# Kernel optimization log

Measured on AMD Instinct MI355X. Metric: run time of the kernel, lower is better.

## Reference

```python
import jax, jax.numpy as jnp
import numpy as np

EPS = 1e-8  # torch F.cosine_similarity eps


def setup_inputs() -> dict:
    key = jax.random.key(0)
    k1, k2 = jax.random.split(key)
    B, D = 8192, 512
    return {
        "label_tensor": jnp.arange(B, dtype=jnp.int64),
        "feature_a": jax.random.normal(k1, (B, D), dtype=jnp.float32),
        "feature_b": jax.random.normal(k2, (B, D), dtype=jnp.float32),
        "affine_w": jnp.ones((1,), dtype=jnp.float32),   # AffineModel scale
        "affine_b": jnp.zeros((1,), dtype=jnp.float32),  # AffineModel bias
    }


def reference(label_tensor, feature_a, feature_b, affine_w, affine_b):
    # cos_score[i, j] = cos(a_i, b_j): normalize then one [B,D]x[D,B] GEMM
    a_n = feature_a / jnp.maximum(
        jnp.linalg.norm(feature_a, axis=1, keepdims=True), EPS)
    b_n = feature_b / jnp.maximum(
        jnp.linalg.norm(feature_b, axis=1, keepdims=True), EPS)
    cos_score = jnp.einsum("id,jd->ij", a_n, b_n)  # [B, B]
    cos_score = affine_w[0] * cos_score + affine_b[0]  # AffineModel
    # cross-entropy with labels = arange(B) -> diagonal of log_softmax
    logp = jax.nn.log_softmax(cos_score, axis=1)
    B = cos_score.shape[0]
    loss = -jnp.mean(logp[jnp.arange(B), jnp.arange(B)])
    return (loss, cos_score)
```

## Files before the change

kernel.cpp:

```cpp
#include <hip/hip_runtime.h>
#include <hip/hip_bf16.h>

#define B_ROWS 8192
#define DIM 512

typedef __bf16 bf16x8 __attribute__((ext_vector_type(8)));
typedef float f32x4 __attribute__((ext_vector_type(4)));

__device__ inline ushort f2bf(float x) {
    __hip_bfloat16 h = __float2bfloat16(x);
    return __builtin_bit_cast(ushort, h);
}

__global__ __launch_bounds__(256) void norm_kernel(const float* __restrict__ A,
                                                   const float* __restrict__ Bf,
                                                   ushort* __restrict__ An,
                                                   ushort* __restrict__ Bn) {
    int gw = (blockIdx.x * 256 + threadIdx.x) >> 6;
    int lane = threadIdx.x & 63;
    const float* src;
    ushort* dst;
    if (gw < B_ROWS) {
        src = A + (size_t)gw * DIM;
        dst = An + (size_t)gw * DIM;
    } else {
        src = Bf + (size_t)(gw - B_ROWS) * DIM;
        dst = Bn + (size_t)(gw - B_ROWS) * DIM;
    }
    const float4* s4 = (const float4*)src;
    float4 v0 = s4[lane * 2];
    float4 v1 = s4[lane * 2 + 1];
    float ss = v0.x * v0.x + v0.y * v0.y + v0.z * v0.z + v0.w * v0.w
             + v1.x * v1.x + v1.y * v1.y + v1.z * v1.z + v1.w * v1.w;
#pragma unroll
    for (int m = 32; m >= 1; m >>= 1) ss += __shfl_xor(ss, m, 64);
    float scale = 1.0f / fmaxf(sqrtf(ss), 1e-8f);
    union { ushort us[8]; uint4 q; } o;
    o.us[0] = f2bf(v0.x * scale); o.us[1] = f2bf(v0.y * scale);
    o.us[2] = f2bf(v0.z * scale); o.us[3] = f2bf(v0.w * scale);
    o.us[4] = f2bf(v1.x * scale); o.us[5] = f2bf(v1.y * scale);
    o.us[6] = f2bf(v1.z * scale); o.us[7] = f2bf(v1.w * scale);
    ((uint4*)dst)[lane] = o.q;
}

__global__ __launch_bounds__(256, 2) void gemm_kernel(
    const ushort* __restrict__ An, const ushort* __restrict__ Bn,
    float* __restrict__ C, float* __restrict__ row_sum,
    const float* __restrict__ wp, const float* __restrict__ bp) {
    __shared__ ushort lds[8192];

    const int t = threadIdx.x;
    const int brow = blockIdx.y * 128;
    const int bcol = blockIdx.x * 128;
    const int wid = t >> 6, lane = t & 63;
    const int wr = wid >> 1, wc = wid & 1;

    const int sr = t >> 2;
    const int sc = (t & 3) * 8;
    const ushort* gA = An + (size_t)(brow + sr) * DIM + sc;
    const ushort* gB = Bn + (size_t)(bcol + sr) * DIM + sc;
    ushort* lA = &lds[t * 8];
    ushort* lB = &lds[4096 + t * 8];

    f32x4 acc[4][4];
#pragma unroll
    for (int i = 0; i < 4; i++)
#pragma unroll
        for (int j = 0; j < 4; j++) acc[i][j] = (f32x4){0.f, 0.f, 0.f, 0.f};

    const int fr = lane & 15;
    const int fk = (lane >> 4) * 8;

    for (int kt = 0; kt < DIM / 32; ++kt) {
        const int k0 = kt * 32;
        __syncthreads();
        __builtin_amdgcn_global_load_lds(
            (const __attribute__((address_space(1))) unsigned int*)(gA + k0),
            (__attribute__((address_space(3))) unsigned int*)lA, 16, 0, 0);
        __builtin_amdgcn_global_load_lds(
            (const __attribute__((address_space(1))) unsigned int*)(gA + (size_t)64 * DIM + k0),
            (__attribute__((address_space(3))) unsigned int*)(lA + 2048), 16, 0, 0);
        __builtin_amdgcn_global_load_lds(
            (const __attribute__((address_space(1))) unsigned int*)(gB + k0),
            (__attribute__((address_space(3))) unsigned int*)lB, 16, 0, 0);
        __builtin_amdgcn_global_load_lds(
            (const __attribute__((address_space(1))) unsigned int*)(gB + (size_t)64 * DIM + k0),
            (__attribute__((address_space(3))) unsigned int*)(lB + 2048), 16, 0, 0);
        __syncthreads();

        bf16x8 af[4], bfr[4];
#pragma unroll
        for (int m = 0; m < 4; ++m) {
            int row = wr * 64 + m * 16 + fr;
            af[m] = *(const bf16x8*)&lds[row * 32 + fk];
        }
#pragma unroll
        for (int n = 0; n < 4; ++n) {
            int col = wc * 64 + n * 16 + fr;
            bfr[n] = *(const bf16x8*)&lds[4096 + col * 32 + fk];
        }
#pragma unroll
        for (int m = 0; m < 4; ++m)
#pragma unroll
            for (int n = 0; n < 4; ++n)
                acc[m][n] = __builtin_amdgcn_mfma_f32_16x16x32_bf16(af[m], bfr[n], acc[m][n], 0, 0, 0);
    }

    const float w = wp[0], bb = bp[0];
    const float M = fabsf(w) + fabsf(bb);
#pragma unroll
    for (int m = 0; m < 4; ++m) {
#pragma unroll
        for (int r = 0; r < 4; ++r) {
            int grow = brow + wr * 64 + m * 16 + (lane >> 4) * 4 + r;
            float psum = 0.f;
#pragma unroll
            for (int n = 0; n < 4; ++n) {
                int gcol = bcol + wc * 64 + n * 16 + (lane & 15);
                float s = w * acc[m][n][r] + bb;
                C[(size_t)grow * B_ROWS + gcol] = s;
                psum += __expf(s - M);
            }
#pragma unroll
            for (int msk = 1; msk <= 8; msk <<= 1) psum += __shfl_xor(psum, msk, 64);
            if ((lane & 15) == 0) atomicAdd(&row_sum[grow], psum);
        }
    }
}

__global__ __launch_bounds__(1024) void loss_kernel(const float* __restrict__ C,
                                                    const float* __restrict__ row_sum,
                                                    const float* __restrict__ wp,
                                                    const float* __restrict__ bp,
                                                    float* __restrict__ out0) {
    __shared__ float sred[16];
    float M = fabsf(wp[0]) + fabsf(bp[0]);
    float local = 0.f;
    for (int i = threadIdx.x; i < B_ROWS; i += 1024) {
        float sii = C[(size_t)i * (B_ROWS + 1)];
        local += sii - M - __logf(row_sum[i]);
    }
#pragma unroll
    for (int m = 32; m >= 1; m >>= 1) local += __shfl_xor(local, m, 64);
    if ((threadIdx.x & 63) == 0) sred[threadIdx.x >> 6] = local;
    __syncthreads();
    if (threadIdx.x == 0) {
        float tot = 0.f;
        for (int i = 0; i < 16; ++i) tot += sred[i];
        out0[0] = -tot / (float)B_ROWS;
    }
}

extern "C" void kernel_launch(void* const* d_in, const int* in_sizes, int n_in,
                              void* d_out, int out_size, void* d_ws, size_t ws_size,
                              hipStream_t stream) {
    const float* A  = (const float*)d_in[1];
    const float* Bf = (const float*)d_in[2];
    const float* wp = (const float*)d_in[3];
    const float* bp = (const float*)d_in[4];
    float* out = (float*)d_out;

    ushort* An = (ushort*)d_ws;
    ushort* Bn = An + (size_t)B_ROWS * DIM;
    float* row_sum = (float*)((char*)d_ws + (size_t)2 * B_ROWS * DIM * sizeof(ushort));

    hipMemsetAsync(row_sum, 0, B_ROWS * sizeof(float), stream);
    norm_kernel<<<dim3(16384 * 64 / 256), 256, 0, stream>>>(A, Bf, An, Bn);
    dim3 grid(B_ROWS / 128, B_ROWS / 128);
    gemm_kernel<<<grid, 256, 0, stream>>>(An, Bn, out + 1, row_sum, wp, bp);
    loss_kernel<<<1, 1024, 0, stream>>>(out + 1, row_sum, wp, bp, out);
}
```

Measured before the change: 437.2 us.

## Use 256x256 double-buffered swizzled GEMM tiles and deterministic row-sum partials

Enlarges the GEMM block tile to 256x256 with 512 threads and double-buffers the LDS tiles, prefetching the next k-slice while MFMAs run. It adds an XOR swizzle on LDS chunks to cut bank conflicts and raises wave priority around the MFMA block. Per-row exp sums are reduced in shared memory and written as per-column-block partials instead of using global atomics. The loss kernel then runs across many blocks and combines results with one atomic per block. The cost is more registers and LDS per block, which may lower occupancy, plus an extra partials buffer.

Measured after the change: 397.7 us. 9.0% less time.

```diff
diff --git a/kernel.cpp b/kernel.cpp
--- a/kernel.cpp
+++ b/kernel.cpp
@@ -43,111 +43,121 @@
     ((uint4*)dst)[lane] = o.q;
 }
 
-__global__ __launch_bounds__(256, 2) void gemm_kernel(
+#define GLDS(src, dst) __builtin_amdgcn_global_load_lds( \
+    (const __attribute__((address_space(1))) unsigned int*)(src), \
+    (__attribute__((address_space(3))) unsigned int*)(dst), 16, 0, 0)
+
+__global__ __launch_bounds__(512, 2) void gemm_kernel(
     const ushort* __restrict__ An, const ushort* __restrict__ Bn,
-    float* __restrict__ C, float* __restrict__ row_sum,
+    float* __restrict__ C, float* __restrict__ rowpart,
     const float* __restrict__ wp, const float* __restrict__ bp) {
-    __shared__ ushort lds[8192];
+    __shared__ ushort ldsA[2][8192];
+    __shared__ ushort ldsB[2][8192];
 
     const int t = threadIdx.x;
-    const int brow = blockIdx.y * 128;
-    const int bcol = blockIdx.x * 128;
+    const int brow = blockIdx.y * 256;
+    const int bcol = blockIdx.x * 256;
     const int wid = t >> 6, lane = t & 63;
-    const int wr = wid >> 1, wc = wid & 1;
+    const int wr = wid >> 2, wc = wid & 3;
+    const int fr = lane & 15;
+    const int fhi = lane >> 4;
 
-    const int sr = t >> 2;
-    const int sc = (t & 3) * 8;
-    const ushort* gA = An + (size_t)(brow + sr) * DIM + sc;
-    const ushort* gB = Bn + (size_t)(bcol + sr) * DIM + sc;
-    ushort* lA = &lds[t * 8];
-    ushort* lB = &lds[4096 + t * 8];
+    const int srow = t >> 2;
+    const int schunk = (t & 3) ^ ((t >> 3) & 3);
+    const ushort* gA0 = An + (size_t)(brow + srow) * DIM + schunk * 8;
+    const ushort* gA1 = gA0 + (size_t)128 * DIM;
+    const ushort* gB0 = Bn + (size_t)(bcol + srow) * DIM + schunk * 8;
+    const ushort* gB1 = gB0 + (size_t)128 * DIM;
 
-    f32x4 acc[4][4];
+#define STAGE(buf, kt) do { const int k0_ = (kt) * 32;            \
+        GLDS(gA0 + k0_, &ldsA[buf][t * 8]);                       \
+        GLDS(gA1 + k0_, &ldsA[buf][4096 + t * 8]);                \
+        GLDS(gB0 + k0_, &ldsB[buf][t * 8]);                       \
+        GLDS(gB1 + k0_, &ldsB[buf][4096 + t * 8]); } while (0)
+
+    f32x4 acc[8][4];
 #pragma unroll
-    for (int i = 0; i < 4; i++)
+    for (int i = 0; i < 8; i++)
 #pragma unroll
         for (int j = 0; j < 4; j++) acc[i][j] = (f32x4){0.f, 0.f, 0.f, 0.f};
 
-    const int fr = lane & 15;
-    const int fk = (lane >> 4) * 8;
+    const int rchunk = (fhi ^ ((fr >> 1) & 3)) * 8;
 
-    for (int kt = 0; kt < DIM / 32; ++kt) {
-        const int k0 = kt * 32;
-        __syncthreads();
-        __builtin_amdgcn_global_load_lds(
-            (const __attribute__((address_space(1))) unsigned int*)(gA + k0),
-            (__attribute__((address_space(3))) unsigned int*)lA, 16, 0, 0);
-        __builtin_amdgcn_global_load_lds(
-            (const __attribute__((address_space(1))) unsigned int*)(gA + (size_t)64 * DIM + k0),
-            (__attribute__((address_space(3))) unsigned int*)(lA + 2048), 16, 0, 0);
-        __builtin_amdgcn_global_load_lds(
-            (const __attribute__((address_space(1))) unsigned int*)(gB + k0),
-            (__attribute__((address_space(3))) unsigned int*)lB, 16, 0, 0);
-        __builtin_amdgcn_global_load_lds(
-            (const __attribute__((address_space(1))) unsigned int*)(gB + (size_t)64 * DIM + k0),
-            (__attribute__((address_space(3))) unsigned int*)(lB + 2048), 16, 0, 0);
-        __syncthreads();
+    STAGE(0, 0);
+    __syncthreads();
 
-        bf16x8 af[4], bfr[4];
+    int cur = 0;
 #pragma unroll
-        for (int m = 0; m < 4; ++m) {
-            int row = wr * 64 + m * 16 + fr;
-            af[m] = *(const bf16x8*)&lds[row * 32 + fk];
-        }
+    for (int kt = 0; kt < 16; ++kt) {
+        if (kt < 15) STAGE(cur ^ 1, kt + 1);
+        bf16x8 af[8], bfr[4];
 #pragma unroll
-        for (int n = 0; n < 4; ++n) {
-            int col = wc * 64 + n * 16 + fr;
-            bfr[n] = *(const bf16x8*)&lds[4096 + col * 32 + fk];
-        }
+        for (int m = 0; m < 8; ++m)
+            af[m] = *(const bf16x8*)&ldsA[cur][(wr * 128 + m * 16 + fr) * 32 + rchunk];
 #pragma unroll
-        for (int m = 0; m < 4; ++m)
+        for (int n = 0; n < 4; ++n)
+            bfr[n] = *(const bf16x8*)&ldsB[cur][(wc * 64 + n * 16 + fr) * 32 + rchunk];
+        __builtin_amdgcn_s_setprio(1);
+#pragma unroll
+        for (int m = 0; m < 8; ++m)
 #pragma unroll
             for (int n = 0; n < 4; ++n)
                 acc[m][n] = __builtin_amdgcn_mfma_f32_16x16x32_bf16(af[m], bfr[n], acc[m][n], 0, 0, 0);
+        __builtin_amdgcn_s_setprio(0);
+        __syncthreads();
+        cur ^= 1;
     }
 
     const float w = wp[0], bb = bp[0];
     const float M = fabsf(w) + fabsf(bb);
+    float* part = (float*)&ldsA[0][0];
 #pragma unroll
-    for (int m = 0; m < 4; ++m) {
+    for (int m = 0; m < 8; ++m) {
 #pragma unroll
         for (int r = 0; r < 4; ++r) {
-            int grow = brow + wr * 64 + m * 16 + (lane >> 4) * 4 + r;
+            const int rloc = wr * 128 + m * 16 + fhi * 4 + r;
+            const size_t grow = (size_t)(brow + rloc);
             float psum = 0.f;
 #pragma unroll
             for (int n = 0; n < 4; ++n) {
-                int gcol = bcol + wc * 64 + n * 16 + (lane & 15);
-                float s = w * acc[m][n][r] + bb;
-                C[(size_t)grow * B_ROWS + gcol] = s;
+                const int gcol = bcol + wc * 64 + n * 16 + fr;
+                float s = fmaf(w, acc[m][n][r], bb);
+                C[grow * B_ROWS + gcol] = s;
                 psum += __expf(s - M);
             }
 #pragma unroll
             for (int msk = 1; msk <= 8; msk <<= 1) psum += __shfl_xor(psum, msk, 64);
-            if ((lane & 15) == 0) atomicAdd(&row_sum[grow], psum);
+            if (fr == 0) part[wc * 256 + rloc] = psum;
         }
     }
+    __syncthreads();
+    if (t < 256) {
+        float s = part[t] + part[256 + t] + part[512 + t] + part[768 + t];
+        rowpart[(size_t)blockIdx.x * B_ROWS + brow + t] = s;
+    }
+#undef STAGE
 }
 
-__global__ __launch_bounds__(1024) void loss_kernel(const float* __restrict__ C,
-                                                    const float* __restrict__ row_sum,
-                                                    const float* __restrict__ wp,
-                                                    const float* __restrict__ bp,
-                                                    float* __restrict__ out0) {
-    __shared__ float sred[16];
-    float M = fabsf(wp[0]) + fabsf(bp[0]);
-    float local = 0.f;
-    for (int i = threadIdx.x; i < B_ROWS; i += 1024) {
-        float sii = C[(size_t)i * (B_ROWS + 1)];
-        local += sii - M - __logf(row_sum[i]);
-    }
+__global__ __launch_bounds__(256) void loss_kernel(const float* __restrict__ C,
+                                                   const float* __restrict__ rowpart,
+                                                   const float* __restrict__ wp,
+                                                   const float* __restrict__ bp,
+                                                   float* __restrict__ out0) {
+    __shared__ float sred[4];
+    const int row = blockIdx.x * 256 + threadIdx.x;
+    float rs = 0.f;
 #pragma unroll
-    for (int m = 32; m >= 1; m >>= 1) local += __shfl_xor(local, m, 64);
-    if ((threadIdx.x & 63) == 0) sred[threadIdx.x >> 6] = local;
+    for (int j = 0; j < 32; ++j) rs += rowpart[(size_t)j * B_ROWS + row];
+    const float M = fabsf(wp[0]) + fabsf(bp[0]);
+    const float sii = C[(size_t)row * B_ROWS + row];
+    float v = sii - M - __logf(rs);
+#pragma unroll
+    for (int msk = 32; msk >= 1; msk >>= 1) v += __shfl_xor(v, msk, 64);
+    if ((threadIdx.x & 63) == 0) sred[threadIdx.x >> 6] = v;
     __syncthreads();
     if (threadIdx.x == 0) {
-        float tot = 0.f;
-        for (int i = 0; i < 16; ++i) tot += sred[i];
-        out0[0] = -tot / (float)B_ROWS;
+        float tot = sred[0] + sred[1] + sred[2] + sred[3];
+        atomicAdd(out0, -tot / (float)B_ROWS);
     }
 }
 
@@ -162,11 +172,11 @@
 
     ushort* An = (ushort*)d_ws;
     ushort* Bn = An + (size_t)B_ROWS * DIM;
-    float* row_sum = (float*)((char*)d_ws + (size_t)2 * B_ROWS * DIM * sizeof(ushort));
+    float* rowpart = (float*)((char*)d_ws + (size_t)2 * B_ROWS * DIM * sizeof(ushort));
 
-    hipMemsetAsync(row_sum, 0, B_ROWS * sizeof(float), stream);
+    hipMemsetAsync(d_out, 0, sizeof(float), stream);
     norm_kernel<<<dim3(16384 * 64 / 256), 256, 0, stream>>>(A, Bf, An, Bn);
-    dim3 grid(B_ROWS / 128, B_ROWS / 128);
-    gemm_kernel<<<grid, 256, 0, stream>>>(An, Bn, out + 1, row_sum, wp, bp);
-    loss_kernel<<<1, 1024, 0, stream>>>(out + 1, row_sum, wp, bp, out);
+    dim3 grid(B_ROWS / 256, B_ROWS / 256);
+    gemm_kernel<<<grid, 512, 0, stream>>>(An, Bn, out + 1, rowpart, wp, bp);
+    loss_kernel<<<B_ROWS / 256, 256, 0, stream>>>(out + 1, rowpart, wp, bp, out);
 }
```
